# Kernel tuning notes

Hardware: AMD Instinct MI355X
Metric: run time of the kernel (lower is better)

The kernel has to match this reference:

```python
import jax, jax.numpy as jnp
import numpy as np

B = 1024
U = 2048

def setup_inputs() -> dict:
    key = jax.random.key(0)
    k1, k2, k3, k4 = jax.random.split(key, 4)
    x = jax.random.normal(k1, (B, U), dtype=jnp.float32)
    h = jax.random.normal(k2, (B, U), dtype=jnp.float32)
    c = jax.random.normal(k3, (B, U), dtype=jnp.float32)
    # keras 'uniform' initializer ~ U(-0.05, 0.05); scale similarly
    w = jax.random.uniform(k4, (2 * U, 4 * U), dtype=jnp.float32, minval=-0.05, maxval=0.05)
    return {"x": x, "h": h, "c": c, "w": w}

def reference(x, h, c, w):
    # concat -> matmul -> split into 4 gates -> gating
    xh = jnp.concatenate([x, h], axis=1)            # [B, 2U]
    ifgo = xh @ w                                   # [B, 4U]
    i, f, g, o = jnp.split(ifgo, 4, axis=1)
    i = jax.nn.sigmoid(i)
    f = jax.nn.sigmoid(f)
    o = jax.nn.sigmoid(o)
    g = jnp.tanh(g)
    c_new = f * c + i * g
    h_new = o * jnp.tanh(c_new)
    return (h_new, h_new, c_new)
```

## Files before the change

kernel.cpp:

```cpp
#include <hip/hip_runtime.h>


#define BDIM   1024
#define UDIM   2048
#define KDIM   4096
#define NDIM   8192
#define BM 128
#define BK 64
#define NT (KDIM / BK)

typedef __attribute__((ext_vector_type(4))) float        f32x4;
typedef __attribute__((ext_vector_type(8))) short        short8;
typedef __attribute__((ext_vector_type(4))) unsigned int u32x4;

__device__ inline unsigned int cvt_pk_bf16(float lo, float hi) {
    unsigned int r;
    asm("v_cvt_pk_bf16_f32 %0, %1, %2" : "=v"(r) : "v"(lo), "v"(hi));
    return r;
}
__device__ inline float fast_sigmoid(float v) {
    return __builtin_amdgcn_rcpf(1.f + __expf(-v));
}
__device__ inline float fast_tanh(float v) {
    float t = __expf(-2.f * __builtin_fabsf(v));
    float r = (1.f - t) * __builtin_amdgcn_rcpf(1.f + t);
    return __builtin_copysignf(r, v);
}

__global__ __launch_bounds__(256, 2)
void lstm_fused(const float* __restrict__ x, const float* __restrict__ h,
                const float* __restrict__ c, const float* __restrict__ w,
                float* __restrict__ out) {
    __shared__ unsigned short As[2][BM * BK];
    __shared__ unsigned short Bs[2][BM * BK];

    const int tid  = threadIdx.x;
    const int lane = tid & 63;
    const int wid  = tid >> 6;
    const int lrow = lane & 15;
    const int lk   = lane >> 4;

    const int m0 = blockIdx.y * BM;
    const int u0 = blockIdx.x * 32;

    f32x4 acc[2][8];
#pragma unroll
    for (int i = 0; i < 2; ++i)
#pragma unroll
        for (int j = 0; j < 8; ++j)
            acc[i][j] = (f32x4){0.f, 0.f, 0.f, 0.f};

    f32x4 av[4][2];
    float bv[4][8];

    auto loadA = [&](int t) {
        int k0 = t * BK;
        const float* src = (k0 < UDIM) ? x + (size_t)m0 * UDIM + k0
                                       : h + (size_t)m0 * UDIM + (k0 - UDIM);
#pragma unroll
        for (int p = 0; p < 4; ++p) {
            int e = p * 256 + tid, arow = e >> 3, k8 = (e & 7) * 8;
            const float* gp = src + (size_t)arow * UDIM + k8;
            av[p][0] = *(const f32x4*)gp;
            av[p][1] = *(const f32x4*)(gp + 4);
        }
    };
    auto loadB = [&](int t) {
        int k0 = t * BK;
#pragma unroll
        for (int p = 0; p < 4; ++p) {
            int q = p * 256 + tid, np = q & 127, kg = q >> 7;
            int col = (np >> 5) * UDIM + u0 + (np & 31);
            const float* gp = w + (size_t)(k0 + kg * 8) * NDIM + col;
#pragma unroll
            for (int j = 0; j < 8; ++j) bv[p][j] = gp[(size_t)j * NDIM];
        }
    };
    auto writeAB = [&](int buf) {
        char* AsB = (char*)As[buf];
        char* BsB = (char*)Bs[buf];
#pragma unroll
        for (int p = 0; p < 4; ++p) {
            int e = p * 256 + tid, arow = e >> 3, k8 = (e & 7) * 8;
            u32x4 u;
            u[0] = cvt_pk_bf16(av[p][0][0], av[p][0][1]);
            u[1] = cvt_pk_bf16(av[p][0][2], av[p][0][3]);
            u[2] = cvt_pk_bf16(av[p][1][0], av[p][1][1]);
            u[3] = cvt_pk_bf16(av[p][1][2], av[p][1][3]);
            *(u32x4*)(AsB + arow * 128 + ((k8 * 2) ^ ((arow & 7) << 4))) = u;
        }
#pragma unroll
        for (int p = 0; p < 4; ++p) {
            int q = p * 256 + tid, np = q & 127, kg = q >> 7;
            u32x4 u;
#pragma unroll
            for (int j = 0; j < 4; ++j)
                u[j] = cvt_pk_bf16(bv[p][2 * j], bv[p][2 * j + 1]);
            *(u32x4*)(BsB + np * 128 + ((kg * 16) ^ ((np & 7) << 4))) = u;
        }
    };
    auto compute = [&](int buf) {
        const char* AsB = (const char*)As[buf];
        const char* BsB = (const char*)Bs[buf];
#pragma unroll
        for (int kk = 0; kk < 2; ++kk) {
            short8 af[2], bfr[8];
            int kb = kk * 64 + lk * 16;
#pragma unroll
            for (int mi = 0; mi < 2; ++mi) {
                int row = wid * 32 + mi * 16 + lrow;
                af[mi] = *(const short8*)(AsB + row * 128 + (kb ^ ((row & 7) << 4)));
            }
#pragma unroll
            for (int ni = 0; ni < 8; ++ni) {
                int row = ni * 16 + lrow;
                bfr[ni] = *(const short8*)(BsB + row * 128 + (kb ^ ((row & 7) << 4)));
            }
#pragma unroll
            for (int mi = 0; mi < 2; ++mi)
#pragma unroll
                for (int ni = 0; ni < 8; ++ni)
                    acc[mi][ni] = __builtin_amdgcn_mfma_f32_16x16x32_bf16(
                        af[mi], bfr[ni], acc[mi][ni], 0, 0, 0);
        }
    };

    loadA(0); loadB(0);
    writeAB(0);
    loadA(1); loadB(1);
    __syncthreads();

    for (int t = 0; t < NT; ++t) {
        int cur = t & 1;
        if (t + 1 < NT) {
            writeAB(cur ^ 1);
            if (t + 2 < NT) { loadA(t + 2); loadB(t + 2); }
        }
        compute(cur);
        __syncthreads();
    }

    const size_t M = (size_t)BDIM * UDIM;
#pragma unroll
    for (int mi = 0; mi < 2; ++mi) {
        int rbase = m0 + wid * 32 + mi * 16 + lk * 4;
#pragma unroll
        for (int half = 0; half < 2; ++half) {
            int u = u0 + half * 16 + lrow;
            f32x4 iv = acc[mi][0 + half];
            f32x4 fv = acc[mi][2 + half];
            f32x4 gv = acc[mi][4 + half];
            f32x4 ov = acc[mi][6 + half];
#pragma unroll
            for (int r = 0; r < 4; ++r) {
                size_t off = (size_t)(rbase + r) * UDIM + u;
                float cc = fast_sigmoid(fv[r]) * c[off] +
                           fast_sigmoid(iv[r]) * fast_tanh(gv[r]);
                float hh = fast_sigmoid(ov[r]) * fast_tanh(cc);
                out[off]         = hh;
                out[M + off]     = hh;
                out[2 * M + off] = cc;
            }
        }
    }
}

extern "C" void kernel_launch(void* const* d_in, const int* in_sizes, int n_in,
                              void* d_out, int out_size, void* d_ws, size_t ws_size,
                              hipStream_t stream) {
    const float* x = (const float*)d_in[0];
    const float* h = (const float*)d_in[1];
    const float* c = (const float*)d_in[2];
    const float* w = (const float*)d_in[3];
    float* out = (float*)d_out;

    dim3 grid(UDIM / 32, BDIM / BM);
    lstm_fused<<<grid, 256, 0, stream>>>(x, h, c, w, out);
}
```

Before: 300.7 us.

## Pre-convert x/h to bf16 workspace and vectorize weight loads

Adds a small pre-pass kernel that concatenates x and h into a bf16 buffer in the workspace, so the GEMM's A loads read half the bytes and skip per-tile conversion. Weight loads change from scalar strided reads to 16-byte vector loads of 4 adjacent columns, with a new LDS swizzle for the B tile's write pattern. MFMA sections are wrapped in s_setprio to favour compute waves. The cost is an extra kernel launch plus a workspace write and read of the concatenated activations.

```diff
diff --git a/kernel.cpp b/kernel.cpp
--- a/kernel.cpp
+++ b/kernel.cpp
@@ -27,10 +27,27 @@
     return __builtin_copysignf(r, v);
 }
 
+__global__ __launch_bounds__(256)
+void concat_bf16(const float* __restrict__ x, const float* __restrict__ h,
+                 unsigned short* __restrict__ xhb) {
+    int idx = blockIdx.x * 256 + threadIdx.x;
+    int r = idx >> 9;
+    int g = idx & 511;
+    const float* src = (g < 256) ? x + (size_t)r * UDIM + g * 8
+                                 : h + (size_t)r * UDIM + (g - 256) * 8;
+    f32x4 a = *(const f32x4*)src;
+    f32x4 b = *(const f32x4*)(src + 4);
+    u32x4 u;
+    u[0] = cvt_pk_bf16(a[0], a[1]);
+    u[1] = cvt_pk_bf16(a[2], a[3]);
+    u[2] = cvt_pk_bf16(b[0], b[1]);
+    u[3] = cvt_pk_bf16(b[2], b[3]);
+    *(u32x4*)(xhb + (size_t)r * KDIM + g * 8) = u;
+}
+
 __global__ __launch_bounds__(256, 2)
-void lstm_fused(const float* __restrict__ x, const float* __restrict__ h,
-                const float* __restrict__ c, const float* __restrict__ w,
-                float* __restrict__ out) {
+void lstm_fused(const unsigned short* __restrict__ xhb, const float* __restrict__ c,
+                const float* __restrict__ w, float* __restrict__ out) {
     __shared__ unsigned short As[2][BM * BK];
     __shared__ unsigned short Bs[2][BM * BK];
 
@@ -43,6 +60,13 @@
     const int m0 = blockIdx.y * BM;
     const int u0 = blockIdx.x * 32;
 
+    const int ar_base = wid * 8 + (lane >> 3);
+    const int ac      = lane & 7;
+    const int nq  = tid & 31;
+    const int kg  = tid >> 5;
+    const int np0 = nq * 4;
+    const int bcol = (np0 >> 5) * UDIM + u0 + (np0 & 31);
+
     f32x4 acc[2][8];
 #pragma unroll
     for (int i = 0; i < 2; ++i)
@@ -50,53 +74,41 @@
         for (int j = 0; j < 8; ++j)
             acc[i][j] = (f32x4){0.f, 0.f, 0.f, 0.f};
 
-    f32x4 av[4][2];
-    float bv[4][8];
+    u32x4 avq[4];
+    f32x4 bvv[8];
 
     auto loadA = [&](int t) {
-        int k0 = t * BK;
-        const float* src = (k0 < UDIM) ? x + (size_t)m0 * UDIM + k0
-                                       : h + (size_t)m0 * UDIM + (k0 - UDIM);
 #pragma unroll
         for (int p = 0; p < 4; ++p) {
-            int e = p * 256 + tid, arow = e >> 3, k8 = (e & 7) * 8;
-            const float* gp = src + (size_t)arow * UDIM + k8;
-            av[p][0] = *(const f32x4*)gp;
-            av[p][1] = *(const f32x4*)(gp + 4);
+            int row = p * 32 + ar_base;
+            avq[p] = *(const u32x4*)(xhb + (size_t)(m0 + row) * KDIM + t * BK + ac * 8);
         }
     };
     auto loadB = [&](int t) {
-        int k0 = t * BK;
+        const float* gp = w + (size_t)(t * BK + kg * 8) * NDIM + bcol;
+#pragma unroll
+        for (int j = 0; j < 8; ++j)
+            bvv[j] = *(const f32x4*)(gp + (size_t)j * NDIM);
+    };
+    auto writeA = [&](int buf) {
+        char* AsB = (char*)As[buf];
 #pragma unroll
         for (int p = 0; p < 4; ++p) {
-            int q = p * 256 + tid, np = q & 127, kg = q >> 7;
-            int col = (np >> 5) * UDIM + u0 + (np & 31);
-            const float* gp = w + (size_t)(k0 + kg * 8) * NDIM + col;
-#pragma unroll
-            for (int j = 0; j < 8; ++j) bv[p][j] = gp[(size_t)j * NDIM];
+            int row = p * 32 + ar_base;
+            *(u32x4*)(AsB + row * 128 + ((ac ^ (row & 7)) << 4)) = avq[p];
         }
     };
-    auto writeAB = [&](int buf) {
-        char* AsB = (char*)As[buf];
+    auto writeB = [&](int buf) {
         char* BsB = (char*)Bs[buf];
 #pragma unroll
-        for (int p = 0; p < 4; ++p) {
-            int e = p * 256 + tid, arow = e >> 3, k8 = (e & 7) * 8;
-            u32x4 u;
-            u[0] = cvt_pk_bf16(av[p][0][0], av[p][0][1]);
-            u[1] = cvt_pk_bf16(av[p][0][2], av[p][0][3]);
-            u[2] = cvt_pk_bf16(av[p][1][0], av[p][1][1]);
-            u[3] = cvt_pk_bf16(av[p][1][2], av[p][1][3]);
-            *(u32x4*)(AsB + arow * 128 + ((k8 * 2) ^ ((arow & 7) << 4))) = u;
-        }
-#pragma unroll
-        for (int p = 0; p < 4; ++p) {
-            int q = p * 256 + tid, np = q & 127, kg = q >> 7;
+        for (int d = 0; d < 4; ++d) {
+            int row = np0 + d;
             u32x4 u;
 #pragma unroll
-            for (int j = 0; j < 4; ++j)
-                u[j] = cvt_pk_bf16(bv[p][2 * j], bv[p][2 * j + 1]);
-            *(u32x4*)(BsB + np * 128 + ((kg * 16) ^ ((np & 7) << 4))) = u;
+            for (int jj = 0; jj < 4; ++jj)
+                u[jj] = cvt_pk_bf16(bvv[2 * jj][d], bvv[2 * jj + 1][d]);
+            int ch = kg ^ ((row ^ (row >> 2)) & 7);
+            *(u32x4*)(BsB + row * 128 + (ch << 4)) = u;
         }
     };
     auto compute = [&](int buf) {
@@ -105,35 +117,38 @@
 #pragma unroll
         for (int kk = 0; kk < 2; ++kk) {
             short8 af[2], bfr[8];
-            int kb = kk * 64 + lk * 16;
+            int cd = kk * 4 + lk;
 #pragma unroll
             for (int mi = 0; mi < 2; ++mi) {
                 int row = wid * 32 + mi * 16 + lrow;
-                af[mi] = *(const short8*)(AsB + row * 128 + (kb ^ ((row & 7) << 4)));
+                af[mi] = *(const short8*)(AsB + row * 128 + ((cd ^ (row & 7)) << 4));
             }
 #pragma unroll
             for (int ni = 0; ni < 8; ++ni) {
                 int row = ni * 16 + lrow;
-                bfr[ni] = *(const short8*)(BsB + row * 128 + (kb ^ ((row & 7) << 4)));
+                bfr[ni] = *(const short8*)(BsB + row * 128 +
+                                           ((cd ^ ((row ^ (row >> 2)) & 7)) << 4));
             }
+            __builtin_amdgcn_s_setprio(1);
 #pragma unroll
             for (int mi = 0; mi < 2; ++mi)
 #pragma unroll
                 for (int ni = 0; ni < 8; ++ni)
                     acc[mi][ni] = __builtin_amdgcn_mfma_f32_16x16x32_bf16(
                         af[mi], bfr[ni], acc[mi][ni], 0, 0, 0);
+            __builtin_amdgcn_s_setprio(0);
         }
     };
 
     loadA(0); loadB(0);
-    writeAB(0);
+    writeA(0); writeB(0);
     loadA(1); loadB(1);
     __syncthreads();
 
     for (int t = 0; t < NT; ++t) {
         int cur = t & 1;
         if (t + 1 < NT) {
-            writeAB(cur ^ 1);
+            writeA(cur ^ 1); writeB(cur ^ 1);
             if (t + 2 < NT) { loadA(t + 2); loadB(t + 2); }
         }
         compute(cur);
@@ -172,8 +187,11 @@
     const float* h = (const float*)d_in[1];
     const float* c = (const float*)d_in[2];
     const float* w = (const float*)d_in[3];
+    unsigned short* xhb = (unsigned short*)d_ws;
     float* out = (float*)d_out;
 
+    concat_bf16<<<(BDIM * KDIM / 8) / 256, 256, 0, stream>>>(x, h, xhb);
+
     dim3 grid(UDIM / 32, BDIM / BM);
-    lstm_fused<<<grid, 256, 0, stream>>>(x, h, c, w, out);
+    lstm_fused<<<grid, 256, 0, stream>>>(xhb, c, w, out);
 }
```

Result: no change. 301.0 us (+0.1%).
